# Optimization experiments

Hardware: AMD Instinct MI355X
Metric: run time of the kernel (lower is better)

Reference implementation:

```python
import jax, jax.numpy as jnp
import numpy as np

EPS = 1e-5


def hetero_layernorm(x, node_type, gamma, beta):
    # LayerNorm over feature dim with per-node-type affine params.
    mu = jnp.mean(x, axis=-1, keepdims=True)
    var = jnp.mean(jnp.square(x - mu), axis=-1, keepdims=True)
    xn = (x - mu) * jax.lax.rsqrt(var + EPS)
    return xn * gamma[node_type] + beta[node_type]


def rgcn_conv(y, edge_src, edge_dst, edge_type, W_rel, W_root):
    # Transform per relation first (R small), then gather per-edge message.
    n = y.shape[0]
    h = jnp.einsum('nd,rde->rne', y, W_rel)          # [R, N, d]
    msg = h[edge_type, edge_src]                     # [E, d] gather
    agg = jax.ops.segment_sum(msg, edge_dst, num_segments=n)  # [N, d]
    return agg + y @ W_root


def hetero_mlp(y, node_type, W_mlp, b_mlp):
    # Per-node-type linear: compute for all T types, then select.
    n = y.shape[0]
    h = jnp.einsum('nd,tde->tne', y, W_mlp) + b_mlp[:, None, :]  # [T, N, d]
    return h[node_type, jnp.arange(n)]


def setup_inputs() -> dict:
    key = jax.random.key(0)
    ks = jax.random.split(key, 8)
    N, E, D, T, R = 50000, 800000, 128, 4, 8
    x = jax.random.normal(ks[0], (N, D), dtype=jnp.float32)
    edge_src = jax.random.randint(ks[1], (E,), 0, N, dtype=jnp.int32)
    edge_dst = jax.random.randint(ks[2], (E,), 0, N, dtype=jnp.int32)
    node_type = jax.random.randint(ks[3], (N,), 0, T, dtype=jnp.int32)
    edge_type = jax.random.randint(ks[4], (E,), 0, R, dtype=jnp.int32)
    # Scale weights ~ 1/sqrt(fan_in) for stable magnitudes.
    s = 1.0 / np.sqrt(D)
    W_rel = jax.random.normal(ks[5], (R, D, D), dtype=jnp.float32) * s
    W_root = jax.random.normal(ks[6], (D, D), dtype=jnp.float32) * s
    W_mlp = jax.random.normal(ks[7], (T, D, D), dtype=jnp.float32) * s
    return {
        'x': x, 'edge_src': edge_src, 'edge_dst': edge_dst,
        'node_type': node_type, 'edge_type': edge_type,
        'conv_gamma': jnp.ones((T, D), jnp.float32),
        'conv_beta': jnp.zeros((T, D), jnp.float32),
        'W_rel': W_rel, 'W_root': W_root,
        'mlp_gamma': jnp.ones((T, D), jnp.float32),
        'mlp_beta': jnp.zeros((T, D), jnp.float32),
        'W_mlp': W_mlp, 'b_mlp': jnp.zeros((T, D), jnp.float32),
    }


def reference(x, edge_src, edge_dst, node_type, edge_type,
              conv_gamma, conv_beta, W_rel, W_root,
              mlp_gamma, mlp_beta, W_mlp, b_mlp):
    # Norm -> Act -> (Dropout p=0, eval) -> Conv -> Residual
    y = hetero_layernorm(x, node_type, conv_gamma, conv_beta)
    y = jax.nn.relu(y)
    x = x + rgcn_conv(y, edge_src, edge_dst, edge_type, W_rel, W_root)
    # Norm -> Act -> (Dropout p=0, eval) -> MLP -> Residual
    y = hetero_layernorm(x, node_type, mlp_gamma, mlp_beta)
    y = jax.nn.relu(y)
    x = x + hetero_mlp(y, node_type, W_mlp, b_mlp)
    return x
```

## Files before the change

kernel.cpp:

```cpp
#include <hip/hip_runtime.h>
#include <hip/hip_bf16.h>

#define D 128
#define EPS 1e-5f
#define CHK 8192
#define P2CAP 6144

typedef __attribute__((ext_vector_type(8))) short short8;
typedef __attribute__((ext_vector_type(4))) float float4v;

#define AS1 __attribute__((address_space(1)))
#define AS3 __attribute__((address_space(3)))

__device__ inline ushort f2bf(float f) {
    __hip_bfloat16 b = __float2bfloat16(f);
    return *reinterpret_cast<ushort*>(&b);
}
__device__ inline float bf_lo(uint u) { return __uint_as_float(u << 16); }
__device__ inline float bf_hi(uint u) { return __uint_as_float(u & 0xffff0000u); }

__global__ void k_ln1cvt(const float* __restrict__ x, const int* __restrict__ ntp,
                         const float* __restrict__ gamma, const float* __restrict__ beta,
                         ushort* __restrict__ y,
                         const float* __restrict__ Wrel, const float* __restrict__ Wroot,
                         const float* __restrict__ Wmlp, ushort* __restrict__ Wt,
                         const int* __restrict__ edst, int* __restrict__ hist,
                         int N, int E, int C, int B) {
    __shared__ ushort t[128][136];
    __shared__ int cnt[256];
    if (blockIdx.x < 13) {
        int m = blockIdx.x;
        const float* src = (m == 0) ? Wroot
                         : (m <= 8) ? Wrel + (size_t)(m - 1) * D * D
                                    : Wmlp + (size_t)(m - 9) * D * D;
        for (int i = threadIdx.x; i < D * D; i += 256) {
            int k = i >> 7, n = i & 127;
            t[n][k] = f2bf(src[i]);
        }
        __syncthreads();
        ushort* dst = Wt + (size_t)m * D * D;
        for (int i = threadIdx.x; i < D * D; i += 256) {
            int frag = i >> 9;
            int lane = (i >> 3) & 63;
            int j = i & 7;
            int nt = frag >> 2, ks = frag & 3;
            int n = nt * 16 + (lane & 15);
            int k = ks * 32 + (lane >> 4) * 8 + j;
            dst[i] = t[n][k];
        }
        return;
    }
    int c = blockIdx.x - 13;
    if (c < C) {
        int tid = threadIdx.x;
        cnt[tid] = 0;
        __syncthreads();
        #pragma unroll 4
        for (int k = 0; k < CHK / 256; ++k) {
            int e = c * CHK + k * 256 + tid;
            if (e < E) atomicAdd(&cnt[edst[e] >> 8], 1);
        }
        __syncthreads();
        if (tid < B) hist[c * B + tid] = cnt[tid];
    }
    int n = (blockIdx.x - 13) * 4 + (threadIdx.x >> 6);
    if (n >= N) return;
    int l = threadIdx.x & 63;
    float2 v = *(const float2*)(x + (size_t)n * D + 2 * l);
    float s = v.x + v.y, s2 = v.x * v.x + v.y * v.y;
    #pragma unroll
    for (int o = 32; o; o >>= 1) { s += __shfl_xor(s, o, 64); s2 += __shfl_xor(s2, o, 64); }
    float mu = s * (1.0f / D);
    float var = s2 * (1.0f / D) - mu * mu;
    float inv = rsqrtf(var + EPS);
    int tt = ntp[n];
    float2 g = *(const float2*)(gamma + tt * D + 2 * l);
    float2 b = *(const float2*)(beta + tt * D + 2 * l);
    float a0 = fmaxf((v.x - mu) * inv * g.x + b.x, 0.0f);
    float a1 = fmaxf((v.y - mu) * inv * g.y + b.y, 0.0f);
    ((uint*)(y + (size_t)n * D))[l] = ((uint)f2bf(a1) << 16) | f2bf(a0);
}

__global__ void k_c2(const int* __restrict__ hist, int* __restrict__ chunkoff,
                     int* __restrict__ bucktot, int C, int B) {
    __shared__ int v[128];
    int b = blockIdx.x, t = threadIdx.x;
    v[t] = (t < C) ? hist[t * B + b] : 0;
    __syncthreads();
    if (t == 0) {
        int s = 0;
        for (int c = 0; c < C; ++c) { int x = v[c]; v[c] = s; s += x; }
        bucktot[b] = s;
    }
    __syncthreads();
    if (t < C) chunkoff[t * B + b] = v[t];
}
__global__ void k_p1s(const int* __restrict__ edst, const int* __restrict__ esrc,
                      const int* __restrict__ etyp, const int* __restrict__ bucktot,
                      const int* __restrict__ chunkoff, uint* __restrict__ edata,
                      int E, int B) {
    __shared__ int ps[256];
    __shared__ int base[256];
    __shared__ int cnt[256];
    int c = blockIdx.x, tid = threadIdx.x;
    int bt = (tid < B) ? bucktot[tid] : 0;
    ps[tid] = bt;
    __syncthreads();
    for (int o = 1; o < 256; o <<= 1) {
        int v = (tid >= o) ? ps[tid - o] : 0;
        __syncthreads();
        ps[tid] += v;
        __syncthreads();
    }
    base[tid] = (ps[tid] - bt) + ((tid < B) ? chunkoff[c * B + tid] : 0);
    cnt[tid] = 0;
    __syncthreads();
    #pragma unroll 4
    for (int k = 0; k < CHK / 256; ++k) {
        int e = c * CHK + k * 256 + tid;
        if (e < E) {
            int d = edst[e];
            int b = d >> 8;
            int r = atomicAdd(&cnt[b], 1);
            edata[base[b] + r] =
                ((uint)esrc[e] << 12) | ((uint)(d & 255) << 4) | (uint)etyp[e];
        }
    }
}
__global__ void k_p2(const uint* __restrict__ edata, const int* __restrict__ bucktot,
                     uint* __restrict__ epack, int* __restrict__ offs,
                     int N, int E, int B) {
    __shared__ int ps[256];
    __shared__ uint ed[P2CAP];
    __shared__ int cnt[256], off[256], cur[256];
    int b = blockIdx.x, tid = threadIdx.x;
    int bt = (tid < B) ? bucktot[tid] : 0;
    ps[tid] = bt;
    __syncthreads();
    for (int o = 1; o < 256; o <<= 1) {
        int v = (tid >= o) ? ps[tid - o] : 0;
        __syncthreads();
        ps[tid] += v;
        __syncthreads();
    }
    int j0 = ps[b] - ((b < B) ? bucktot[b] : 0);
    int count = ps[b] - j0;
    if (count > P2CAP) count = P2CAP;
    for (int i = tid; i < count; i += 256) ed[i] = edata[j0 + i];
    cnt[tid] = 0;
    __syncthreads();
    for (int i = tid; i < count; i += 256) atomicAdd(&cnt[(ed[i] >> 4) & 255], 1);
    __syncthreads();
    int myc = cnt[tid];
    ps[tid] = myc;
    __syncthreads();
    for (int o = 1; o < 256; o <<= 1) {
        int v = (tid >= o) ? ps[tid - o] : 0;
        __syncthreads();
        ps[tid] += v;
        __syncthreads();
    }
    off[tid] = ps[tid] - myc;
    cur[tid] = ps[tid] - myc;
    __syncthreads();
    for (int i = tid; i < count; i += 256) {
        uint v = ed[i];
        int dl = (v >> 4) & 255;
        int r = atomicAdd(&cur[dl], 1);
        epack[j0 + r] = ((v & 15u) << 28) | (v >> 12);
    }
    int v = b * 256 + tid;
    if (v < N) offs[v] = j0 + off[tid];
    if (b == 0 && tid == 0) offs[N] = E;
}

__global__ void k_zagg(const ushort* __restrict__ ybuf, const int* __restrict__ offs,
                       const uint* __restrict__ epack, ushort* __restrict__ zbuf, int N) {
    int wave = threadIdx.x >> 6;
    int l = threadIdx.x & 63;
    int v = blockIdx.x * 4 + wave;
    if (v >= N) return;
    float2 a0 = {0.f,0.f}, a1 = {0.f,0.f}, a2 = {0.f,0.f}, a3 = {0.f,0.f};
    float2 a4 = {0.f,0.f}, a5 = {0.f,0.f}, a6 = {0.f,0.f}, a7 = {0.f,0.f};
    const uint* yb = (const uint*)ybuf;
    int j = offs[v], e1 = offs[v + 1];

#define ZACC(P, U) do {                                                   \
        float lo = bf_lo(U), hi = bf_hi(U);                               \
        switch ((P) >> 28) {                                              \
            case 0: a0.x += lo; a0.y += hi; break;                        \
            case 1: a1.x += lo; a1.y += hi; break;                        \
            case 2: a2.x += lo; a2.y += hi; break;                        \
            case 3: a3.x += lo; a3.y += hi; break;                        \
            case 4: a4.x += lo; a4.y += hi; break;                        \
            case 5: a5.x += lo; a5.y += hi; break;                        \
            case 6: a6.x += lo; a6.y += hi; break;                        \
            default: a7.x += lo; a7.y += hi; break;                       \
        }                                                                 \
    } while (0)

    while (j < e1) {
        int chunk = min(64, e1 - j);
        uint pl = (j + l < e1) ? epack[j + l] : 0;
        int i = 0;
        for (; i + 3 < chunk; i += 4) {
            uint p0 = __shfl(pl, i, 64);
            uint p1 = __shfl(pl, i + 1, 64);
            uint p2 = __shfl(pl, i + 2, 64);
            uint p3 = __shfl(pl, i + 3, 64);
            uint u0 = yb[(size_t)(p0 & 0x0FFFFFFFu) * 64 + l];
            uint u1 = yb[(size_t)(p1 & 0x0FFFFFFFu) * 64 + l];
            uint u2 = yb[(size_t)(p2 & 0x0FFFFFFFu) * 64 + l];
            uint u3 = yb[(size_t)(p3 & 0x0FFFFFFFu) * 64 + l];
            ZACC(p0, u0); ZACC(p1, u1); ZACC(p2, u2); ZACC(p3, u3);
        }
        for (; i < chunk; ++i) {
            uint p = __shfl(pl, i, 64);
            uint u = yb[(size_t)(p & 0x0FFFFFFFu) * 64 + l];
            ZACC(p, u);
        }
        j += chunk;
    }
#undef ZACC
    uint* zrow = (uint*)(zbuf + (size_t)v * 1024);
    zrow[0 * 64 + l] = ((uint)f2bf(a0.y) << 16) | f2bf(a0.x);
    zrow[1 * 64 + l] = ((uint)f2bf(a1.y) << 16) | f2bf(a1.x);
    zrow[2 * 64 + l] = ((uint)f2bf(a2.y) << 16) | f2bf(a2.x);
    zrow[3 * 64 + l] = ((uint)f2bf(a3.y) << 16) | f2bf(a3.x);
    zrow[4 * 64 + l] = ((uint)f2bf(a4.y) << 16) | f2bf(a4.x);
    zrow[5 * 64 + l] = ((uint)f2bf(a5.y) << 16) | f2bf(a5.x);
    zrow[6 * 64 + l] = ((uint)f2bf(a6.y) << 16) | f2bf(a6.x);
    zrow[7 * 64 + l] = ((uint)f2bf(a7.y) << 16) | f2bf(a7.x);
}

__device__ __forceinline__ void gl_lds16(const void* g, void* l) {
    __builtin_amdgcn_global_load_lds((const AS1 void*)g, (AS3 void*)l, 16, 0, 0);
}
__device__ __forceinline__ void stage_half(const ushort* __restrict__ Wt, int q,
                                           ushort* bsm0, int wave, int lane) {
    const char* g = (const char*)Wt + (size_t)q * 16384 + lane * 16;
    char* l = (char*)bsm0 + (q & 1) * 16384;
    #pragma unroll
    for (int i = 0; i < 4; ++i) {
        int c = i * 4 + wave;
        gl_lds16(g + c * 1024, l + c * 1024);
    }
}
__device__ __forceinline__ void stage_mlp_slice(const ushort* __restrict__ Wt, int nt,
                                                ushort* bsm0, int wave, int lane) {
    const char* g = (const char*)Wt + (size_t)(9 + wave) * 32768 + nt * 4096 + lane * 16;
    char* l = (char*)bsm0 + (nt & 1) * 16384 + wave * 4096;
    #pragma unroll
    for (int i = 0; i < 4; ++i)
        gl_lds16(g + i * 1024, l + i * 1024);
}
__device__ __forceinline__ void aloadG(short8 (&d)[4], const ushort* p, int off, int ao) {
    #pragma unroll
    for (int ks = 0; ks < 4; ++ks)
        d[ks] = *(const short8*)(p + off + ks * 32 + ao);
}
__device__ __forceinline__ void convHalf(float4v (&acc)[8], const short8 (&a)[4],
                                         const ushort* bsm_h, int h, int lane) {
    #pragma unroll
    for (int nt4 = 0; nt4 < 4; ++nt4) {
        #pragma unroll
        for (int ks = 0; ks < 4; ++ks) {
            short8 b = *(const short8*)(bsm_h + (((nt4 * 4 + ks) * 64 + lane) << 3));
            acc[h * 4 + nt4] = __builtin_amdgcn_mfma_f32_16x16x32_bf16(
                a[ks], b, acc[h * 4 + nt4], 0, 0, 0);
        }
    }
}

__launch_bounds__(256, 4)
__global__ void k_gm(const ushort* __restrict__ ybuf, const ushort* __restrict__ zbuf,
                     const ushort* __restrict__ Wt, const float* __restrict__ x,
                     const int* __restrict__ ntp,
                     const float* __restrict__ gamma, const float* __restrict__ beta,
                     const float* __restrict__ bmlp, float* __restrict__ out, int N) {
    __shared__ ushort bsm[2][8192];
    ushort* bsm0 = &bsm[0][0];
    int tid = threadIdx.x;
    int wave = tid >> 6, lane = tid & 63;
    int quad = lane >> 4, l15 = lane & 15;
    int ao = quad * 8;
    int base = blockIdx.x * 64 + wave * 16;

    const ushort* yrow = ybuf + (size_t)min(base + l15, N - 1) * 128;
    const ushort* zrow = zbuf + (size_t)min(base + l15, N - 1) * 1024;

    float4v acc[8];
    #pragma unroll
    for (int nt = 0; nt < 8; ++nt) acc[nt] = (float4v){0.f, 0.f, 0.f, 0.f};

    short8 aC[4], aN[4];
    stage_half(Wt, 0, bsm0, wave, lane);
    aloadG(aC, yrow, 0, ao);
    __syncthreads();

    #pragma unroll
    for (int m = 0; m < 9; ++m) {
        short8 (&cur)[4] = (m & 1) ? aN : aC;
        short8 (&nxt)[4] = (m & 1) ? aC : aN;
        stage_half(Wt, 2 * m + 1, bsm0, wave, lane);
        if (m < 8) aloadG(nxt, zrow, m * 128, ao);
        convHalf(acc, cur, bsm0, 0, lane);
        __syncthreads();
        if (m < 8) stage_half(Wt, 2 * m + 2, bsm0, wave, lane);
        else       stage_mlp_slice(Wt, 0, bsm0, wave, lane);
        convHalf(acc, cur, bsm0 + 8192, 1, lane);
        __syncthreads();
    }

    ushort* yov = bsm0 + 8192 + wave * 2048;
    int ty[4];
    {
        float s[4] = {0.f, 0.f, 0.f, 0.f}, s2[4] = {0.f, 0.f, 0.f, 0.f};
        #pragma unroll
        for (int nt = 0; nt < 8; ++nt) {
            int col = nt * 16 + l15;
            #pragma unroll
            for (int r = 0; r < 4; ++r) {
                int row = base + quad * 4 + r;
                float xv = (row < N) ? x[(size_t)row * D + col] : 0.f;
                float t = acc[nt][r] + xv;
                acc[nt][r] = t;
                s[r] += t; s2[r] += t * t;
            }
        }
        #pragma unroll
        for (int r = 0; r < 4; ++r) {
            #pragma unroll
            for (int o = 1; o < 16; o <<= 1) {
                s[r]  += __shfl_xor(s[r],  o, 64);
                s2[r] += __shfl_xor(s2[r], o, 64);
            }
        }
        #pragma unroll
        for (int r = 0; r < 4; ++r) {
            int rc = min(base + quad * 4 + r, N - 1);
            ty[r] = ntp[rc];
            float mu  = s[r] * (1.0f / D);
            float var = s2[r] * (1.0f / D) - mu * mu;
            float inv = rsqrtf(var + EPS);
            int lrow = quad * 4 + r;
            #pragma unroll
            for (int nt = 0; nt < 8; ++nt) {
                int col = nt * 16 + l15;
                float yn = fmaxf((acc[nt][r] - mu) * inv * gamma[ty[r] * D + col]
                                 + beta[ty[r] * D + col], 0.f);
                yov[lrow * 128 + col] = f2bf(yn);
            }
        }
    }
    short8 a2[4];
    {
        const ushort* myrow = yov + l15 * 128;
        #pragma unroll
        for (int ks = 0; ks < 4; ++ks) a2[ks] = *(const short8*)(myrow + ks * 32 + ao);
    }
    __syncthreads();

    #pragma unroll
    for (int nt = 0; nt < 8; ++nt) {
        if (nt < 7) stage_mlp_slice(Wt, nt + 1, bsm0, wave, lane);
        const ushort* bh = bsm0 + (nt & 1) * 8192;
        float4v c0 = {0.f,0.f,0.f,0.f}, c1 = {0.f,0.f,0.f,0.f};
        float4v c2 = {0.f,0.f,0.f,0.f}, c3 = {0.f,0.f,0.f,0.f};
        #pragma unroll
        for (int ks = 0; ks < 4; ++ks) {
            int fo = (ks * 64 + lane) << 3;
            short8 b0 = *(const short8*)(bh + 0 * 2048 + fo);
            short8 b1 = *(const short8*)(bh + 1 * 2048 + fo);
            short8 b2 = *(const short8*)(bh + 2 * 2048 + fo);
            short8 b3 = *(const short8*)(bh + 3 * 2048 + fo);
            c0 = __builtin_amdgcn_mfma_f32_16x16x32_bf16(a2[ks], b0, c0, 0, 0, 0);
            c1 = __builtin_amdgcn_mfma_f32_16x16x32_bf16(a2[ks], b1, c1, 0, 0, 0);
            c2 = __builtin_amdgcn_mfma_f32_16x16x32_bf16(a2[ks], b2, c2, 0, 0, 0);
            c3 = __builtin_amdgcn_mfma_f32_16x16x32_bf16(a2[ks], b3, c3, 0, 0, 0);
        }
        int col = nt * 16 + l15;
        #pragma unroll
        for (int r = 0; r < 4; ++r) {
            int row = base + quad * 4 + r;
            if (row < N) {
                int t = ty[r];
                float v = (t == 0) ? c0[r] : (t == 1) ? c1[r] : (t == 2) ? c2[r] : c3[r];
                out[(size_t)row * D + col] = acc[nt][r] + v + bmlp[t * D + col];
            }
        }
        if (nt < 7) __syncthreads();
    }
}

extern "C" void kernel_launch(void* const* d_in, const int* in_sizes, int n_in,
                              void* d_out, int out_size, void* d_ws, size_t ws_size,
                              hipStream_t stream) {
    const float* x          = (const float*)d_in[0];
    const int*   esrc       = (const int*)d_in[1];
    const int*   edst       = (const int*)d_in[2];
    const int*   ntyp       = (const int*)d_in[3];
    const int*   etyp       = (const int*)d_in[4];
    const float* conv_gamma = (const float*)d_in[5];
    const float* conv_beta  = (const float*)d_in[6];
    const float* W_rel      = (const float*)d_in[7];
    const float* W_root     = (const float*)d_in[8];
    const float* mlp_gamma  = (const float*)d_in[9];
    const float* mlp_beta   = (const float*)d_in[10];
    const float* W_mlp      = (const float*)d_in[11];
    const float* b_mlp      = (const float*)d_in[12];
    float* out = (float*)d_out;

    int N = in_sizes[0] / D;
    int E = in_sizes[1];
    int C = (E + CHK - 1) / CHK;
    int B = (N + 255) / 256;

    char* p = (char*)d_ws;
    auto take = [&p](size_t bytes) { char* q = p; p += (bytes + 255) & ~(size_t)255; return q; };
    ushort* ybuf    = (ushort*)take((size_t)N * D * 2);
    ushort* zbuf    = (ushort*)take((size_t)N * 1024 * 2);
    ushort* Wt      = (ushort*)take((size_t)13 * D * D * 2);
    uint*   edata   = (uint*)take((size_t)E * 4);
    uint*   epack   = (uint*)take((size_t)E * 4);
    int*    offs    = (int*)take((size_t)(N + 1) * 4);
    int*    hist    = (int*)take((size_t)C * B * 4);
    int*    chunkoff= (int*)take((size_t)C * B * 4);
    int*    bucktot = (int*)take((size_t)B * 4);

    k_ln1cvt<<<13 + (N + 3) / 4, 256, 0, stream>>>(x, ntyp, conv_gamma, conv_beta,
                                                   ybuf, W_rel, W_root, W_mlp, Wt,
                                                   edst, hist, N, E, C, B);

    k_c2<<<B, 128, 0, stream>>>(hist, chunkoff, bucktot, C, B);
    k_p1s<<<C, 256, 0, stream>>>(edst, esrc, etyp, bucktot, chunkoff, edata, E, B);
    k_p2<<<B, 256, 0, stream>>>(edata, bucktot, epack, offs, N, E, B);

    k_zagg<<<(N + 3) / 4, 256, 0, stream>>>(ybuf, offs, epack, zbuf, N);

    k_gm<<<(N + 63) / 64, 256, 0, stream>>>(ybuf, zbuf, Wt, x, ntyp,
                                            mlp_gamma, mlp_beta, b_mlp, out, N);
}
```

Baseline: 253.1 us.

## Transform per relation before gather instead of aggregating per-relation neighbor sums

Switches the RGCN computation order. A new kernel k_h first computes h[r] = y·W_rel[r] for all 8 relations and stores them as bf16. The aggregation kernel then gathers the already-transformed rows and sums them into a single 128-wide vector per node, instead of building per-relation 1024-wide sums. The fused GEMM kernel now only multiplies by W_root and adds the aggregated messages in its epilogue, which shrinks its K dimension from 1152 to 128. The trade-off is extra traffic: writing the [8,N,128] h buffer (about 100MB), plus an additional bf16 rounding of each message before it is summed.

```diff
diff --git a/kernel.cpp b/kernel.cpp
--- a/kernel.cpp
+++ b/kernel.cpp
@@ -174,31 +174,96 @@
     if (b == 0 && tid == 0) offs[N] = E;
 }
 
-__global__ void k_zagg(const ushort* __restrict__ ybuf, const int* __restrict__ offs,
-                       const uint* __restrict__ epack, ushort* __restrict__ zbuf, int N) {
+__device__ __forceinline__ void gl_lds16(const void* g, void* l) {
+    __builtin_amdgcn_global_load_lds((const AS1 void*)g, (AS3 void*)l, 16, 0, 0);
+}
+__device__ __forceinline__ void stage_half(const ushort* __restrict__ Wt, int q,
+                                           ushort* bsm0, int wave, int lane) {
+    const char* g = (const char*)Wt + (size_t)q * 16384 + lane * 16;
+    char* l = (char*)bsm0 + (q & 1) * 16384;
+    #pragma unroll
+    for (int i = 0; i < 4; ++i) {
+        int c = i * 4 + wave;
+        gl_lds16(g + c * 1024, l + c * 1024);
+    }
+}
+__device__ __forceinline__ void stage_mlp_slice(const ushort* __restrict__ Wt, int nt,
+                                                ushort* bsm0, int wave, int lane) {
+    const char* g = (const char*)Wt + (size_t)(9 + wave) * 32768 + nt * 4096 + lane * 16;
+    char* l = (char*)bsm0 + (nt & 1) * 16384 + wave * 4096;
+    #pragma unroll
+    for (int i = 0; i < 4; ++i)
+        gl_lds16(g + i * 1024, l + i * 1024);
+}
+__device__ __forceinline__ void aloadG(short8 (&d)[4], const ushort* p, int off, int ao) {
+    #pragma unroll
+    for (int ks = 0; ks < 4; ++ks)
+        d[ks] = *(const short8*)(p + off + ks * 32 + ao);
+}
+__device__ __forceinline__ void convHalf(float4v (&acc)[8], const short8 (&a)[4],
+                                         const ushort* bsm_h, int h, int lane) {
+    #pragma unroll
+    for (int nt4 = 0; nt4 < 4; ++nt4) {
+        #pragma unroll
+        for (int ks = 0; ks < 4; ++ks) {
+            short8 b = *(const short8*)(bsm_h + (((nt4 * 4 + ks) * 64 + lane) << 3));
+            acc[h * 4 + nt4] = __builtin_amdgcn_mfma_f32_16x16x32_bf16(
+                a[ks], b, acc[h * 4 + nt4], 0, 0, 0);
+        }
+    }
+}
+
+__launch_bounds__(256, 4)
+__global__ void k_h(const ushort* __restrict__ ybuf, const ushort* __restrict__ Wt,
+                    ushort* __restrict__ h, int N) {
+    __shared__ ushort bsm[2][8192];
+    ushort* bsm0 = &bsm[0][0];
+    int tid = threadIdx.x;
+    int wave = tid >> 6, lane = tid & 63;
+    int quad = lane >> 4, l15 = lane & 15;
+    int ao = quad * 8;
+    int base = blockIdx.x * 64 + wave * 16;
+    const ushort* yrow = ybuf + (size_t)min(base + l15, N - 1) * 128;
+
+    short8 aY[4];
+    aloadG(aY, yrow, 0, ao);
+    stage_half(Wt, 2, bsm0, wave, lane);
+    __syncthreads();
+
+    #pragma unroll
+    for (int r = 0; r < 8; ++r) {
+        float4v acc[8];
+        #pragma unroll
+        for (int nt = 0; nt < 8; ++nt) acc[nt] = (float4v){0.f, 0.f, 0.f, 0.f};
+        stage_half(Wt, 3 + 2 * r, bsm0, wave, lane);
+        convHalf(acc, aY, bsm0, 0, lane);
+        __syncthreads();
+        if (r < 7) stage_half(Wt, 4 + 2 * r, bsm0, wave, lane);
+        convHalf(acc, aY, bsm0 + 8192, 1, lane);
+        #pragma unroll
+        for (int nt = 0; nt < 8; ++nt) {
+            int col = nt * 16 + l15;
+            #pragma unroll
+            for (int rr = 0; rr < 4; ++rr) {
+                int row = base + quad * 4 + rr;
+                if (row < N)
+                    h[((size_t)r * N + row) * 128 + col] = f2bf(acc[nt][rr]);
+            }
+        }
+        __syncthreads();
+    }
+}
+
+__global__ void k_zagg(const ushort* __restrict__ h, const int* __restrict__ offs,
+                       const uint* __restrict__ epack, ushort* __restrict__ agg, int N) {
     int wave = threadIdx.x >> 6;
     int l = threadIdx.x & 63;
     int v = blockIdx.x * 4 + wave;
     if (v >= N) return;
     float2 a0 = {0.f,0.f}, a1 = {0.f,0.f}, a2 = {0.f,0.f}, a3 = {0.f,0.f};
-    float2 a4 = {0.f,0.f}, a5 = {0.f,0.f}, a6 = {0.f,0.f}, a7 = {0.f,0.f};
-    const uint* yb = (const uint*)ybuf;
+    const uint* hb = (const uint*)h;
+    size_t Ns = (size_t)N;
     int j = offs[v], e1 = offs[v + 1];
-
-#define ZACC(P, U) do {                                                   \
-        float lo = bf_lo(U), hi = bf_hi(U);                               \
-        switch ((P) >> 28) {                                              \
-            case 0: a0.x += lo; a0.y += hi; break;                        \
-            case 1: a1.x += lo; a1.y += hi; break;                        \
-            case 2: a2.x += lo; a2.y += hi; break;                        \
-            case 3: a3.x += lo; a3.y += hi; break;                        \
-            case 4: a4.x += lo; a4.y += hi; break;                        \
-            case 5: a5.x += lo; a5.y += hi; break;                        \
-            case 6: a6.x += lo; a6.y += hi; break;                        \
-            default: a7.x += lo; a7.y += hi; break;                       \
-        }                                                                 \
-    } while (0)
-
     while (j < e1) {
         int chunk = min(64, e1 - j);
         uint pl = (j + l < e1) ? epack[j + l] : 0;
@@ -208,72 +273,29 @@
             uint p1 = __shfl(pl, i + 1, 64);
             uint p2 = __shfl(pl, i + 2, 64);
             uint p3 = __shfl(pl, i + 3, 64);
-            uint u0 = yb[(size_t)(p0 & 0x0FFFFFFFu) * 64 + l];
-            uint u1 = yb[(size_t)(p1 & 0x0FFFFFFFu) * 64 + l];
-            uint u2 = yb[(size_t)(p2 & 0x0FFFFFFFu) * 64 + l];
-            uint u3 = yb[(size_t)(p3 & 0x0FFFFFFFu) * 64 + l];
-            ZACC(p0, u0); ZACC(p1, u1); ZACC(p2, u2); ZACC(p3, u3);
+            uint u0 = hb[((size_t)(p0 >> 28) * Ns + (p0 & 0x0FFFFFFFu)) * 64 + l];
+            uint u1 = hb[((size_t)(p1 >> 28) * Ns + (p1 & 0x0FFFFFFFu)) * 64 + l];
+            uint u2 = hb[((size_t)(p2 >> 28) * Ns + (p2 & 0x0FFFFFFFu)) * 64 + l];
+            uint u3 = hb[((size_t)(p3 >> 28) * Ns + (p3 & 0x0FFFFFFFu)) * 64 + l];
+            a0.x += bf_lo(u0); a0.y += bf_hi(u0);
+            a1.x += bf_lo(u1); a1.y += bf_hi(u1);
+            a2.x += bf_lo(u2); a2.y += bf_hi(u2);
+            a3.x += bf_lo(u3); a3.y += bf_hi(u3);
         }
         for (; i < chunk; ++i) {
             uint p = __shfl(pl, i, 64);
-            uint u = yb[(size_t)(p & 0x0FFFFFFFu) * 64 + l];
-            ZACC(p, u);
+            uint u = hb[((size_t)(p >> 28) * Ns + (p & 0x0FFFFFFFu)) * 64 + l];
+            a0.x += bf_lo(u); a0.y += bf_hi(u);
         }
         j += chunk;
     }
-#undef ZACC
-    uint* zrow = (uint*)(zbuf + (size_t)v * 1024);
-    zrow[0 * 64 + l] = ((uint)f2bf(a0.y) << 16) | f2bf(a0.x);
-    zrow[1 * 64 + l] = ((uint)f2bf(a1.y) << 16) | f2bf(a1.x);
-    zrow[2 * 64 + l] = ((uint)f2bf(a2.y) << 16) | f2bf(a2.x);
-    zrow[3 * 64 + l] = ((uint)f2bf(a3.y) << 16) | f2bf(a3.x);
-    zrow[4 * 64 + l] = ((uint)f2bf(a4.y) << 16) | f2bf(a4.x);
-    zrow[5 * 64 + l] = ((uint)f2bf(a5.y) << 16) | f2bf(a5.x);
-    zrow[6 * 64 + l] = ((uint)f2bf(a6.y) << 16) | f2bf(a6.x);
-    zrow[7 * 64 + l] = ((uint)f2bf(a7.y) << 16) | f2bf(a7.x);
-}
-
-__device__ __forceinline__ void gl_lds16(const void* g, void* l) {
-    __builtin_amdgcn_global_load_lds((const AS1 void*)g, (AS3 void*)l, 16, 0, 0);
-}
-__device__ __forceinline__ void stage_half(const ushort* __restrict__ Wt, int q,
-                                           ushort* bsm0, int wave, int lane) {
-    const char* g = (const char*)Wt + (size_t)q * 16384 + lane * 16;
-    char* l = (char*)bsm0 + (q & 1) * 16384;
-    #pragma unroll
-    for (int i = 0; i < 4; ++i) {
-        int c = i * 4 + wave;
-        gl_lds16(g + c * 1024, l + c * 1024);
-    }
-}
-__device__ __forceinline__ void stage_mlp_slice(const ushort* __restrict__ Wt, int nt,
-                                                ushort* bsm0, int wave, int lane) {
-    const char* g = (const char*)Wt + (size_t)(9 + wave) * 32768 + nt * 4096 + lane * 16;
-    char* l = (char*)bsm0 + (nt & 1) * 16384 + wave * 4096;
-    #pragma unroll
-    for (int i = 0; i < 4; ++i)
-        gl_lds16(g + i * 1024, l + i * 1024);
-}
-__device__ __forceinline__ void aloadG(short8 (&d)[4], const ushort* p, int off, int ao) {
-    #pragma unroll
-    for (int ks = 0; ks < 4; ++ks)
-        d[ks] = *(const short8*)(p + off + ks * 32 + ao);
-}
-__device__ __forceinline__ void convHalf(float4v (&acc)[8], const short8 (&a)[4],
-                                         const ushort* bsm_h, int h, int lane) {
-    #pragma unroll
-    for (int nt4 = 0; nt4 < 4; ++nt4) {
-        #pragma unroll
-        for (int ks = 0; ks < 4; ++ks) {
-            short8 b = *(const short8*)(bsm_h + (((nt4 * 4 + ks) * 64 + lane) << 3));
-            acc[h * 4 + nt4] = __builtin_amdgcn_mfma_f32_16x16x32_bf16(
-                a[ks], b, acc[h * 4 + nt4], 0, 0, 0);
-        }
-    }
+    float lo = (a0.x + a1.x) + (a2.x + a3.x);
+    float hi = (a0.y + a1.y) + (a2.y + a3.y);
+    ((uint*)agg)[(size_t)v * 64 + l] = ((uint)f2bf(hi) << 16) | f2bf(lo);
 }
 
 __launch_bounds__(256, 4)
-__global__ void k_gm(const ushort* __restrict__ ybuf, const ushort* __restrict__ zbuf,
+__global__ void k_gm(const ushort* __restrict__ ybuf, const ushort* __restrict__ agg,
                      const ushort* __restrict__ Wt, const float* __restrict__ x,
                      const int* __restrict__ ntp,
                      const float* __restrict__ gamma, const float* __restrict__ beta,
@@ -287,30 +309,22 @@
     int base = blockIdx.x * 64 + wave * 16;
 
     const ushort* yrow = ybuf + (size_t)min(base + l15, N - 1) * 128;
-    const ushort* zrow = zbuf + (size_t)min(base + l15, N - 1) * 1024;
 
     float4v acc[8];
     #pragma unroll
     for (int nt = 0; nt < 8; ++nt) acc[nt] = (float4v){0.f, 0.f, 0.f, 0.f};
 
-    short8 aC[4], aN[4];
+    short8 aC[4];
     stage_half(Wt, 0, bsm0, wave, lane);
     aloadG(aC, yrow, 0, ao);
     __syncthreads();
 
-    #pragma unroll
-    for (int m = 0; m < 9; ++m) {
-        short8 (&cur)[4] = (m & 1) ? aN : aC;
-        short8 (&nxt)[4] = (m & 1) ? aC : aN;
-        stage_half(Wt, 2 * m + 1, bsm0, wave, lane);
-        if (m < 8) aloadG(nxt, zrow, m * 128, ao);
-        convHalf(acc, cur, bsm0, 0, lane);
-        __syncthreads();
-        if (m < 8) stage_half(Wt, 2 * m + 2, bsm0, wave, lane);
-        else       stage_mlp_slice(Wt, 0, bsm0, wave, lane);
-        convHalf(acc, cur, bsm0 + 8192, 1, lane);
-        __syncthreads();
-    }
+    stage_half(Wt, 1, bsm0, wave, lane);
+    convHalf(acc, aC, bsm0, 0, lane);
+    __syncthreads();
+    stage_mlp_slice(Wt, 0, bsm0, wave, lane);
+    convHalf(acc, aC, bsm0 + 8192, 1, lane);
+    __syncthreads();
 
     ushort* yov = bsm0 + 8192 + wave * 2048;
     int ty[4];
@@ -322,8 +336,12 @@
             #pragma unroll
             for (int r = 0; r < 4; ++r) {
                 int row = base + quad * 4 + r;
-                float xv = (row < N) ? x[(size_t)row * D + col] : 0.f;
-                float t = acc[nt][r] + xv;
+                float xv = 0.f, av = 0.f;
+                if (row < N) {
+                    xv = x[(size_t)row * D + col];
+                    av = __uint_as_float((uint)agg[(size_t)row * 128 + col] << 16);
+                }
+                float t = acc[nt][r] + xv + av;
                 acc[nt][r] = t;
                 s[r] += t; s2[r] += t * t;
             }
@@ -419,7 +437,8 @@
     char* p = (char*)d_ws;
     auto take = [&p](size_t bytes) { char* q = p; p += (bytes + 255) & ~(size_t)255; return q; };
     ushort* ybuf    = (ushort*)take((size_t)N * D * 2);
-    ushort* zbuf    = (ushort*)take((size_t)N * 1024 * 2);
+    ushort* h       = (ushort*)take((size_t)8 * N * D * 2);
+    ushort* agg     = (ushort*)take((size_t)N * D * 2);
     ushort* Wt      = (ushort*)take((size_t)13 * D * D * 2);
     uint*   edata   = (uint*)take((size_t)E * 4);
     uint*   epack   = (uint*)take((size_t)E * 4);
@@ -432,12 +451,14 @@
                                                    ybuf, W_rel, W_root, W_mlp, Wt,
                                                    edst, hist, N, E, C, B);
 
+    k_h<<<(N + 63) / 64, 256, 0, stream>>>(ybuf, Wt, h, N);
+
     k_c2<<<B, 128, 0, stream>>>(hist, chunkoff, bucktot, C, B);
     k_p1s<<<C, 256, 0, stream>>>(edst, esrc, etyp, bucktot, chunkoff, edata, E, B);
     k_p2<<<B, 256, 0, stream>>>(edata, bucktot, epack, offs, N, E, B);
 
-    k_zagg<<<(N + 3) / 4, 256, 0, stream>>>(ybuf, offs, epack, zbuf, N);
-
-    k_gm<<<(N + 63) / 64, 256, 0, stream>>>(ybuf, zbuf, Wt, x, ntyp,
+    k_zagg<<<(N + 3) / 4, 256, 0, stream>>>(h, offs, epack, agg, N);
+
+    k_gm<<<(N + 63) / 64, 256, 0, stream>>>(ybuf, agg, Wt, x, ntyp,
                                             mlp_gamma, mlp_beta, b_mlp, out, N);
 }
```

Result: slower. 263.0 us (+3.9%).
